# Optimization experiments

Hardware: AMD Instinct MI355X
Metric: run time of the kernel (lower is better)

The kernel has to match this reference:

```python
import jax, jax.numpy as jnp
import numpy as np

B, S, F = 512, 512, 128   # batch, seq_len, facts_size (= querry_size)
H1, H2 = 80, 40
PAD = float(-2**32 + 1)


def setup_inputs() -> dict:
    key = jax.random.key(0)
    ks = jax.random.split(key, 12)
    inp = {
        "query": jax.random.normal(ks[0], (B, F), jnp.float32),
        "facts": jax.random.normal(ks[1], (B, S, F), jnp.float32),
        "mask": jax.random.randint(ks[2], (B, S), 0, 2, jnp.int32),
        # mlp1: querry_size -> facts_size
        "W1": jax.random.normal(ks[3], (F, F), jnp.float32) / np.sqrt(F),
        "b1": jnp.zeros((F,), jnp.float32),
        # PReLU alpha (per-feature, init zeros)
        "alpha": jnp.zeros((F,), jnp.float32),
        # mlp2: 4*F -> 80
        "W2": jax.random.normal(ks[4], (4 * F, H1), jnp.float32) / np.sqrt(4 * F),
        "b2": jnp.zeros((H1,), jnp.float32),
        # mlp3: 80 -> 40
        "W3": jax.random.normal(ks[5], (H1, H2), jnp.float32) / np.sqrt(H1),
        "b3": jnp.zeros((H2,), jnp.float32),
        # mlp4: 40 -> 1
        "W4": jax.random.normal(ks[6], (H2, 1), jnp.float32) / np.sqrt(H2),
        "b4": jnp.zeros((1,), jnp.float32),
    }
    return inp


def reference(query, facts, mask, W1, b1, alpha, W2, b2, W3, b3, W4, b4):
    # mlp1 + PReLU on the query
    q = query @ W1 + b1                                   # [B, F]
    q = jnp.where(q >= 0, q, alpha * q)                   # PReLU, alpha per-feature
    # broadcast query over sequence (tile+reshape in the original)
    qs = jnp.broadcast_to(q[:, None, :], (q.shape[0], S, F))  # [B, S, F]
    din = jnp.concatenate([qs, facts, qs - facts, qs * facts], axis=-1)  # [B,S,4F]
    h1 = jax.nn.sigmoid(din @ W2 + b2)                    # [B, S, 80]
    h2 = jax.nn.sigmoid(h1 @ W3 + b3)                     # [B, S, 40]
    scores = (h2 @ W4 + b4)[..., 0][:, None, :]           # [B, 1, S]
    key_masks = (mask == 1)[:, None, :]                   # [B, 1, S]
    scores = jnp.where(key_masks, scores, PAD)
    scores = jax.nn.softmax(scores, axis=-1)              # softmax over seq
    out = jnp.einsum("bqs,bsf->bqf", scores, facts)       # [B, 1, F]  (mode SUM)
    return out
```

## Files before the change

kernel.cpp:

```cpp
#include <hip/hip_runtime.h>
#include <hip/hip_bf16.h>

typedef __bf16 bf16x8 __attribute__((ext_vector_type(8)));
typedef float  f32x4  __attribute__((ext_vector_type(4)));

#define WBT_STRIDE 136
#define H1_STRIDE  104
#define W3T_STRIDE 104

__global__ __launch_bounds__(512, 4)
void attn_fused(const float* __restrict__ query,
                const float* __restrict__ facts,
                const int*   __restrict__ mask,
                const float* __restrict__ W1, const float* __restrict__ b1,
                const float* __restrict__ alpha,
                const float* __restrict__ W2, const float* __restrict__ b2,
                const float* __restrict__ W3, const float* __restrict__ b3,
                const float* __restrict__ W4,
                float* __restrict__ out)
{
    __shared__ __align__(16) __bf16 WbT[80 * WBT_STRIDE];
    __shared__ __align__(16) __bf16 W3T[48 * W3T_STRIDE];
    __shared__ __align__(16) __bf16 h1all[128 * H1_STRIDE];
    __shared__ float qy[128], qs[128], qcs[80];
    __shared__ float qpart[4][128], qcp[4][80];
    __shared__ float w4s[48], b3s[48];
    __shared__ float outw[8 * 128];
    __shared__ float Zw[8];

    const int b = blockIdx.x, t = threadIdx.x;

    if (t < 128) qy[t] = query[b * 128 + t];
    for (int e = t; e < 48 * 96; e += 512) {
        int j = e / 96, k = e % 96;
        W3T[j * W3T_STRIDE + k] = (j < 40 && k < 80) ? (__bf16)W3[k * 40 + j]
                                                     : (__bf16)0.0f;
    }
    for (int e = t; e < 128 * 16; e += 512) {
        int r = e >> 4, c = 80 + (e & 15);
        h1all[r * H1_STRIDE + c] = (__bf16)0.0f;
    }
    if (t < 48) { w4s[t] = (t < 40) ? W4[t] : 0.f; b3s[t] = (t < 40) ? b3[t] : 0.f; }
    __syncthreads();

    {
        int j = t & 127, kh = t >> 7;
        float acc = (kh == 0) ? b1[j] : 0.f;
        const float* w1p = W1 + (kh * 32) * 128 + j;
        #pragma unroll 8
        for (int k = 0; k < 32; ++k) acc = fmaf(qy[kh * 32 + k], w1p[k * 128], acc);
        qpart[kh][j] = acc;
    }
    __syncthreads();
    if (t < 128) {
        float s = (qpart[0][t] + qpart[1][t]) + (qpart[2][t] + qpart[3][t]);
        qs[t] = (s >= 0.f) ? s : alpha[t] * s;
    }
    __syncthreads();

    if (t < 320) {
        int jj = t % 80, hh = t / 80;
        float acc = (hh == 0) ? b2[jj] : 0.f;
        #pragma unroll 8
        for (int k = hh * 32; k < hh * 32 + 32; ++k)
            acc = fmaf(qs[k], W2[k * 80 + jj] + W2[(256 + k) * 80 + jj], acc);
        qcp[hh][jj] = acc;
    }
    for (int e = t; e < 128 * 80; e += 512) {
        int k = e / 80, n = e - k * 80;
        float w = W2[(128 + k) * 80 + n] - W2[(256 + k) * 80 + n]
                + qs[k] * W2[(384 + k) * 80 + n];
        WbT[n * WBT_STRIDE + k] = (__bf16)w;
    }
    __syncthreads();
    if (t < 80) qcs[t] = (qcp[0][t] + qcp[1][t]) + (qcp[2][t] + qcp[3][t]);
    __syncthreads();

    const int wave = t >> 6, lane = t & 63, qd = lane >> 4, m = lane & 15;
    const float* fb = facts + (size_t)b * (512 * 128);
    const int*   mb = mask + b * 512;
    __bf16* h1w = &h1all[wave * 16 * H1_STRIDE];

    float oacc[4][8];
    #pragma unroll
    for (int kc = 0; kc < 4; ++kc)
        #pragma unroll
        for (int i = 0; i < 8; ++i) oacc[kc][i] = 0.f;
    float Zl = 0.f;

    for (int tile = 0; tile < 4; ++tile) {
        const int s0 = wave * 64 + tile * 16;
        const int mv = mb[s0 + m];

        f32x4 av[4][2];
        {
            const float* p0 = &fb[(size_t)(s0 + m) * 128 + qd * 8];
            #pragma unroll
            for (int kc = 0; kc < 4; ++kc) {
                av[kc][0] = *(const f32x4*)(p0 + kc * 32);
                av[kc][1] = *(const f32x4*)(p0 + kc * 32 + 4);
            }
        }
        bf16x8 af[4];
        #pragma unroll
        for (int kc = 0; kc < 4; ++kc)
            #pragma unroll
            for (int i = 0; i < 8; ++i)
                af[kc][i] = (__bf16)((i < 4) ? av[kc][0][i] : av[kc][1][i - 4]);

        #pragma unroll
        for (int ct = 0; ct < 5; ++ct) {
            f32x4 acc = {0.f, 0.f, 0.f, 0.f};
            #pragma unroll
            for (int kc = 0; kc < 4; ++kc) {
                bf16x8 bfr = *(const bf16x8*)&WbT[(ct * 16 + m) * WBT_STRIDE + kc * 32 + qd * 8];
                acc = __builtin_amdgcn_mfma_f32_16x16x32_bf16(af[kc], bfr, acc, 0, 0, 0);
            }
            const int col = ct * 16 + m;
            const float qc = qcs[col];
            #pragma unroll
            for (int r = 0; r < 4; ++r) {
                float x = acc[r] + qc;
                float h = __builtin_amdgcn_rcpf(1.0f + __expf(-x));
                h1w[(qd * 4 + r) * H1_STRIDE + col] = (__bf16)h;
            }
        }
        asm volatile("s_waitcnt lgkmcnt(0)" ::: "memory");

        bf16x8 a2[3];
        #pragma unroll
        for (int kc = 0; kc < 3; ++kc)
            a2[kc] = *(const bf16x8*)&h1w[m * H1_STRIDE + kc * 32 + qd * 8];
        float sc[4] = {0.f, 0.f, 0.f, 0.f};
        #pragma unroll
        for (int ct = 0; ct < 3; ++ct) {
            f32x4 acc2 = {0.f, 0.f, 0.f, 0.f};
            #pragma unroll
            for (int kc = 0; kc < 3; ++kc) {
                bf16x8 bfr = *(const bf16x8*)&W3T[(ct * 16 + m) * W3T_STRIDE + kc * 32 + qd * 8];
                acc2 = __builtin_amdgcn_mfma_f32_16x16x32_bf16(a2[kc], bfr, acc2, 0, 0, 0);
            }
            const int col = ct * 16 + m;
            const float w4v = w4s[col], b3v = b3s[col];
            #pragma unroll
            for (int r = 0; r < 4; ++r) {
                float h2 = __builtin_amdgcn_rcpf(1.0f + __expf(-(acc2[r] + b3v)));
                sc[r] = fmaf(h2, w4v, sc[r]);
            }
        }
        #pragma unroll
        for (int d = 1; d < 16; d <<= 1)
            #pragma unroll
            for (int r = 0; r < 4; ++r)
                sc[r] += __shfl_xor(sc[r], d);

        const int idx = ((((m >> 2) << 4) | m) << 2);
        float s0v = __int_as_float(__builtin_amdgcn_ds_bpermute(idx, __float_as_int(sc[0])));
        float s1v = __int_as_float(__builtin_amdgcn_ds_bpermute(idx, __float_as_int(sc[1])));
        float s2v = __int_as_float(__builtin_amdgcn_ds_bpermute(idx, __float_as_int(sc[2])));
        float s3v = __int_as_float(__builtin_amdgcn_ds_bpermute(idx, __float_as_int(sc[3])));
        const int rr = m & 3;
        float srow = (rr == 0) ? s0v : (rr == 1) ? s1v : (rr == 2) ? s2v : s3v;

        const float pm = (mv == 1) ? __expf(srow) : 0.f;
        Zl += pm;
        #pragma unroll
        for (int kc = 0; kc < 4; ++kc)
            #pragma unroll
            for (int i = 0; i < 4; ++i) {
                oacc[kc][i]     = fmaf(pm, av[kc][0][i], oacc[kc][i]);
                oacc[kc][i + 4] = fmaf(pm, av[kc][1][i], oacc[kc][i + 4]);
            }
    }

    #pragma unroll
    for (int d = 1; d < 16; d <<= 1) {
        #pragma unroll
        for (int kc = 0; kc < 4; ++kc)
            #pragma unroll
            for (int i = 0; i < 8; ++i)
                oacc[kc][i] += __shfl_xor(oacc[kc][i], d);
        Zl += __shfl_xor(Zl, d);
    }
    if (m == 0) {
        #pragma unroll
        for (int kc = 0; kc < 4; ++kc)
            #pragma unroll
            for (int i = 0; i < 8; ++i)
                outw[wave * 128 + kc * 32 + qd * 8 + i] = oacc[kc][i];
        if (lane == 0) Zw[wave] = Zl;
    }
    __syncthreads();

    if (t < 128) {
        float v = 0.f, Z = 0.f;
        #pragma unroll
        for (int w = 0; w < 8; ++w) { v += outw[w * 128 + t]; Z += Zw[w]; }
        out[b * 128 + t] = v / Z;
    }
}

extern "C" void kernel_launch(void* const* d_in, const int* in_sizes, int n_in,
                              void* d_out, int out_size, void* d_ws, size_t ws_size,
                              hipStream_t stream) {
    (void)in_sizes; (void)n_in; (void)d_ws; (void)ws_size; (void)out_size;
    const float* query = (const float*)d_in[0];
    const float* facts = (const float*)d_in[1];
    const int*   mask  = (const int*)d_in[2];
    const float* W1 = (const float*)d_in[3];
    const float* b1 = (const float*)d_in[4];
    const float* al = (const float*)d_in[5];
    const float* W2 = (const float*)d_in[6];
    const float* b2 = (const float*)d_in[7];
    const float* W3 = (const float*)d_in[8];
    const float* b3 = (const float*)d_in[9];
    const float* W4 = (const float*)d_in[10];
    const float* b4 = (const float*)d_in[11];
    (void)b4;
    attn_fused<<<dim3(512), dim3(512), 0, stream>>>(
        query, facts, mask, W1, b1, al, W2, b2, W3, b3, W4, (float*)d_out);
}
```

Measured before the change: 233.2 us.

## Prefetch facts tiles via register double-buffering and swizzle WbT LDS layout

The first facts tile and all mask values are loaded at kernel start, so they overlap the weight-preprocessing prologue. Inside the now fully unrolled tile loop, the next tile is loaded into a second register buffer and the weighted accumulation for the previous tile is deferred. The WbT LDS layout is XOR-swizzled by row to reduce bank conflicts on the MFMA B-operand reads. This doubles the facts register footprint, which may reduce occupancy under the 512x4 launch bounds or cause spills.

```diff
diff --git a/kernel.cpp b/kernel.cpp
--- a/kernel.cpp
+++ b/kernel.cpp
@@ -29,6 +29,22 @@
     __shared__ float Zw[8];
 
     const int b = blockIdx.x, t = threadIdx.x;
+    const int wave = t >> 6, lane = t & 63, qd = lane >> 4, m = lane & 15;
+    const float* fb = facts + (size_t)b * (512 * 128);
+    const int*   mb = mask + b * 512;
+
+    f32x4 av[2][4][2];
+    int mv[4];
+    {
+        const float* p0 = &fb[(size_t)(wave * 64 + m) * 128 + qd * 8];
+        #pragma unroll
+        for (int kc = 0; kc < 4; ++kc) {
+            av[0][kc][0] = *(const f32x4*)(p0 + kc * 32);
+            av[0][kc][1] = *(const f32x4*)(p0 + kc * 32 + 4);
+        }
+        #pragma unroll
+        for (int tl = 0; tl < 4; ++tl) mv[tl] = mb[wave * 64 + tl * 16 + m];
+    }
 
     if (t < 128) qy[t] = query[b * 128 + t];
     for (int e = t; e < 48 * 96; e += 512) {
@@ -70,15 +86,12 @@
         int k = e / 80, n = e - k * 80;
         float w = W2[(128 + k) * 80 + n] - W2[(256 + k) * 80 + n]
                 + qs[k] * W2[(384 + k) * 80 + n];
-        WbT[n * WBT_STRIDE + k] = (__bf16)w;
+        WbT[n * WBT_STRIDE + (((k >> 3) ^ (n & 3)) << 3) + (k & 7)] = (__bf16)w;
     }
     __syncthreads();
     if (t < 80) qcs[t] = (qcp[0][t] + qcp[1][t]) + (qcp[2][t] + qcp[3][t]);
     __syncthreads();
 
-    const int wave = t >> 6, lane = t & 63, qd = lane >> 4, m = lane & 15;
-    const float* fb = facts + (size_t)b * (512 * 128);
-    const int*   mb = mask + b * 512;
     __bf16* h1w = &h1all[wave * 16 * H1_STRIDE];
 
     float oacc[4][8];
@@ -87,42 +100,54 @@
         #pragma unroll
         for (int i = 0; i < 8; ++i) oacc[kc][i] = 0.f;
     float Zl = 0.f;
-
+    float pmprev = 0.f;
+
+    #pragma unroll
     for (int tile = 0; tile < 4; ++tile) {
-        const int s0 = wave * 64 + tile * 16;
-        const int mv = mb[s0 + m];
-
-        f32x4 av[4][2];
-        {
-            const float* p0 = &fb[(size_t)(s0 + m) * 128 + qd * 8];
+        const int p = tile & 1;
+
+        if (tile > 0) {
+            #pragma unroll
+            for (int kc = 0; kc < 4; ++kc)
+                #pragma unroll
+                for (int i = 0; i < 4; ++i) {
+                    oacc[kc][i]     = fmaf(pmprev, av[1 - p][kc][0][i], oacc[kc][i]);
+                    oacc[kc][i + 4] = fmaf(pmprev, av[1 - p][kc][1][i], oacc[kc][i + 4]);
+                }
+            Zl += pmprev;
+        }
+        if (tile < 3) {
+            const float* pn = &fb[(size_t)(wave * 64 + (tile + 1) * 16 + m) * 128 + qd * 8];
             #pragma unroll
             for (int kc = 0; kc < 4; ++kc) {
-                av[kc][0] = *(const f32x4*)(p0 + kc * 32);
-                av[kc][1] = *(const f32x4*)(p0 + kc * 32 + 4);
-            }
-        }
+                av[1 - p][kc][0] = *(const f32x4*)(pn + kc * 32);
+                av[1 - p][kc][1] = *(const f32x4*)(pn + kc * 32 + 4);
+            }
+        }
+
         bf16x8 af[4];
         #pragma unroll
         for (int kc = 0; kc < 4; ++kc)
             #pragma unroll
             for (int i = 0; i < 8; ++i)
-                af[kc][i] = (__bf16)((i < 4) ? av[kc][0][i] : av[kc][1][i - 4]);
+                af[kc][i] = (__bf16)((i < 4) ? av[p][kc][0][i] : av[p][kc][1][i - 4]);
 
         #pragma unroll
         for (int ct = 0; ct < 5; ++ct) {
             f32x4 acc = {0.f, 0.f, 0.f, 0.f};
+            const int n1 = ct * 16 + m;
             #pragma unroll
             for (int kc = 0; kc < 4; ++kc) {
-                bf16x8 bfr = *(const bf16x8*)&WbT[(ct * 16 + m) * WBT_STRIDE + kc * 32 + qd * 8];
+                bf16x8 bfr = *(const bf16x8*)
+                    &WbT[n1 * WBT_STRIDE + (((kc * 4 + qd) ^ (m & 3)) << 3)];
                 acc = __builtin_amdgcn_mfma_f32_16x16x32_bf16(af[kc], bfr, acc, 0, 0, 0);
             }
-            const int col = ct * 16 + m;
-            const float qc = qcs[col];
+            const float qc = qcs[n1];
             #pragma unroll
             for (int r = 0; r < 4; ++r) {
                 float x = acc[r] + qc;
                 float h = __builtin_amdgcn_rcpf(1.0f + __expf(-x));
-                h1w[(qd * 4 + r) * H1_STRIDE + col] = (__bf16)h;
+                h1w[(qd * 4 + r) * H1_STRIDE + n1] = (__bf16)h;
             }
         }
         asm volatile("s_waitcnt lgkmcnt(0)" ::: "memory");
@@ -162,16 +187,16 @@
         const int rr = m & 3;
         float srow = (rr == 0) ? s0v : (rr == 1) ? s1v : (rr == 2) ? s2v : s3v;
 
-        const float pm = (mv == 1) ? __expf(srow) : 0.f;
-        Zl += pm;
-        #pragma unroll
-        for (int kc = 0; kc < 4; ++kc)
-            #pragma unroll
-            for (int i = 0; i < 4; ++i) {
-                oacc[kc][i]     = fmaf(pm, av[kc][0][i], oacc[kc][i]);
-                oacc[kc][i + 4] = fmaf(pm, av[kc][1][i], oacc[kc][i + 4]);
-            }
-    }
+        pmprev = (mv[tile] == 1) ? __expf(srow) : 0.f;
+    }
+    #pragma unroll
+    for (int kc = 0; kc < 4; ++kc)
+        #pragma unroll
+        for (int i = 0; i < 4; ++i) {
+            oacc[kc][i]     = fmaf(pmprev, av[1][kc][0][i], oacc[kc][i]);
+            oacc[kc][i + 4] = fmaf(pmprev, av[1][kc][1][i], oacc[kc][i + 4]);
+        }
+    Zl += pmprev;
 
     #pragma unroll
     for (int d = 1; d < 16; d <<= 1) {
```

New measurement: 248.5 us. 1.07x slower.

## Split per-batch weight prep into separate kernel and restructure weighted-sum reduction

Applied to the files above, without the earlier changes.

Moves the query MLP, PReLU, folded W2 weight construction and W3 transpose into a prep kernel that writes per-batch bf16 weights to workspace, so the main kernel only copies them into LDS. The main kernel prefetches the first facts tile and the mask before the weight load. It now stores softmax numerators to shared memory and does the weighted sum of facts in a second pass over global memory, replacing the register accumulator and the long shuffle reduction. W3T is read from global instead of LDS. The cost is an extra launch, workspace traffic and a second read of facts, in exchange for less prologue work and lower register and shuffle pressure.

```diff
diff --git a/kernel.cpp b/kernel.cpp
--- a/kernel.cpp
+++ b/kernel.cpp
@@ -3,97 +3,144 @@
 
 typedef __bf16 bf16x8 __attribute__((ext_vector_type(8)));
 typedef float  f32x4  __attribute__((ext_vector_type(4)));
+typedef float  f32x2  __attribute__((ext_vector_type(2)));
 
 #define WBT_STRIDE 136
 #define H1_STRIDE  104
-#define W3T_STRIDE 104
+
+#define WS_WBT   0u
+#define WS_QC    10485760u
+#define WS_W3T   10649600u
+
+__global__ __launch_bounds__(256)
+void k1_prep(const float* __restrict__ query,
+             const float* __restrict__ W1, const float* __restrict__ b1,
+             const float* __restrict__ alpha,
+             const float* __restrict__ W2, const float* __restrict__ b2,
+             const float* __restrict__ W3,
+             unsigned char* __restrict__ ws)
+{
+    __shared__ float qy[128];
+    __shared__ float qpart[2][128];
+    __shared__ float qs[128];
+    __shared__ float qcp[2][80];
+
+    const int b = blockIdx.x, t = threadIdx.x;
+    __hip_bfloat16* wbt = (__hip_bfloat16*)(ws + WS_WBT);
+    float*          qcw = (float*)(ws + WS_QC);
+    __hip_bfloat16* w3t = (__hip_bfloat16*)(ws + WS_W3T);
+
+    if (t < 128) qy[t] = query[b * 128 + t];
+    __syncthreads();
+
+    {
+        const int j = t & 127, kh = t >> 7;
+        float acc = (kh == 0) ? b1[j] : 0.0f;
+        const float* w1p = W1 + (kh * 64) * 128 + j;
+        #pragma unroll 4
+        for (int k = 0; k < 64; ++k) acc = fmaf(qy[kh * 64 + k], w1p[k * 128], acc);
+        qpart[kh][j] = acc;
+    }
+    if (b == 0) {
+        for (int e = t; e < 48 * 96; e += 256) {
+            int j = e / 96, k = e % 96;
+            float v = (j < 40 && k < 80) ? W3[k * 40 + j] : 0.0f;
+            w3t[e] = __hip_bfloat16(v);
+        }
+    }
+    __syncthreads();
+    if (t < 128) {
+        float s = qpart[0][t] + qpart[1][t];
+        float a = alpha[t];
+        qs[t] = (s >= 0.0f) ? s : a * s;
+    }
+    __syncthreads();
+
+    if (t < 160) {
+        const int jj = (t < 80) ? t : t - 80;
+        const int hh = (t < 80) ? 0 : 1;
+        float acc = (hh == 0) ? b2[jj] : 0.0f;
+        #pragma unroll 4
+        for (int k = hh * 64; k < hh * 64 + 64; ++k)
+            acc = fmaf(qs[k], W2[k * 80 + jj] + W2[(256 + k) * 80 + jj], acc);
+        qcp[hh][jj] = acc;
+    }
+    for (int e = t; e < 80 * 16; e += 256) {
+        const int n = e >> 4, c = e & 15;
+        bf16x8 v;
+        #pragma unroll
+        for (int j = 0; j < 8; ++j) {
+            const int k = c * 8 + j;
+            float w = W2[(128 + k) * 80 + n] - W2[(256 + k) * 80 + n]
+                    + qs[k] * W2[(384 + k) * 80 + n];
+            v[j] = (__bf16)w;
+        }
+        *(bf16x8*)&wbt[(size_t)b * 10240 + n * 128 + c * 8] = v;
+    }
+    __syncthreads();
+    if (t < 80) qcw[b * 80 + t] = qcp[0][t] + qcp[1][t];
+}
 
 __global__ __launch_bounds__(512, 4)
-void attn_fused(const float* __restrict__ query,
-                const float* __restrict__ facts,
-                const int*   __restrict__ mask,
-                const float* __restrict__ W1, const float* __restrict__ b1,
-                const float* __restrict__ alpha,
-                const float* __restrict__ W2, const float* __restrict__ b2,
-                const float* __restrict__ W3, const float* __restrict__ b3,
-                const float* __restrict__ W4,
-                float* __restrict__ out)
+void k2_main(const float* __restrict__ facts,
+             const int*   __restrict__ mask,
+             const float* __restrict__ W4, const float* __restrict__ b3,
+             const unsigned char* __restrict__ ws,
+             float* __restrict__ out)
 {
     __shared__ __align__(16) __bf16 WbT[80 * WBT_STRIDE];
-    __shared__ __align__(16) __bf16 W3T[48 * W3T_STRIDE];
     __shared__ __align__(16) __bf16 h1all[128 * H1_STRIDE];
-    __shared__ float qy[128], qs[128], qcs[80];
-    __shared__ float qpart[4][128], qcp[4][80];
+    __shared__ float qcs[80];
     __shared__ float w4s[48], b3s[48];
-    __shared__ float outw[8 * 128];
+    __shared__ float scores[512];
     __shared__ float Zw[8];
 
     const int b = blockIdx.x, t = threadIdx.x;
-
-    if (t < 128) qy[t] = query[b * 128 + t];
-    for (int e = t; e < 48 * 96; e += 512) {
-        int j = e / 96, k = e % 96;
-        W3T[j * W3T_STRIDE + k] = (j < 40 && k < 80) ? (__bf16)W3[k * 40 + j]
-                                                     : (__bf16)0.0f;
+    const int wave = t >> 6, lane = t & 63, qd = lane >> 4, m = lane & 15;
+    const float* fb = facts + (size_t)b * (512 * 128);
+    const int*   mb = mask + b * 512;
+
+    const __hip_bfloat16* wbt_g = (const __hip_bfloat16*)(ws + WS_WBT) + (size_t)b * 10240;
+    const float*          qcw   = (const float*)(ws + WS_QC) + b * 80;
+    const __bf16*         w3t_g = (const __bf16*)(ws + WS_W3T);
+
+    f32x4 av0[4][2];
+    int mv[4];
+    {
+        const float* p0 = &fb[(size_t)(wave * 64 + m) * 128 + qd * 8];
+        #pragma unroll
+        for (int kc = 0; kc < 4; ++kc) {
+            av0[kc][0] = *(const f32x4*)(p0 + kc * 32);
+            av0[kc][1] = *(const f32x4*)(p0 + kc * 32 + 4);
+        }
+        #pragma unroll
+        for (int tl = 0; tl < 4; ++tl) mv[tl] = mb[wave * 64 + tl * 16 + m];
+    }
+
+    for (int e = t; e < 80 * 16; e += 512) {
+        const int n = e >> 4, c = e & 15;
+        bf16x8 v = *(const bf16x8*)&wbt_g[n * 128 + c * 8];
+        *(bf16x8*)&WbT[n * WBT_STRIDE + c * 8] = v;
     }
     for (int e = t; e < 128 * 16; e += 512) {
         int r = e >> 4, c = 80 + (e & 15);
         h1all[r * H1_STRIDE + c] = (__bf16)0.0f;
     }
+    if (t < 80) qcs[t] = qcw[t];
     if (t < 48) { w4s[t] = (t < 40) ? W4[t] : 0.f; b3s[t] = (t < 40) ? b3[t] : 0.f; }
     __syncthreads();
 
-    {
-        int j = t & 127, kh = t >> 7;
-        float acc = (kh == 0) ? b1[j] : 0.f;
-        const float* w1p = W1 + (kh * 32) * 128 + j;
-        #pragma unroll 8
-        for (int k = 0; k < 32; ++k) acc = fmaf(qy[kh * 32 + k], w1p[k * 128], acc);
-        qpart[kh][j] = acc;
-    }
-    __syncthreads();
-    if (t < 128) {
-        float s = (qpart[0][t] + qpart[1][t]) + (qpart[2][t] + qpart[3][t]);
-        qs[t] = (s >= 0.f) ? s : alpha[t] * s;
-    }
-    __syncthreads();
-
-    if (t < 320) {
-        int jj = t % 80, hh = t / 80;
-        float acc = (hh == 0) ? b2[jj] : 0.f;
-        #pragma unroll 8
-        for (int k = hh * 32; k < hh * 32 + 32; ++k)
-            acc = fmaf(qs[k], W2[k * 80 + jj] + W2[(256 + k) * 80 + jj], acc);
-        qcp[hh][jj] = acc;
-    }
-    for (int e = t; e < 128 * 80; e += 512) {
-        int k = e / 80, n = e - k * 80;
-        float w = W2[(128 + k) * 80 + n] - W2[(256 + k) * 80 + n]
-                + qs[k] * W2[(384 + k) * 80 + n];
-        WbT[n * WBT_STRIDE + k] = (__bf16)w;
-    }
-    __syncthreads();
-    if (t < 80) qcs[t] = (qcp[0][t] + qcp[1][t]) + (qcp[2][t] + qcp[3][t]);
-    __syncthreads();
-
-    const int wave = t >> 6, lane = t & 63, qd = lane >> 4, m = lane & 15;
-    const float* fb = facts + (size_t)b * (512 * 128);
-    const int*   mb = mask + b * 512;
     __bf16* h1w = &h1all[wave * 16 * H1_STRIDE];
 
-    float oacc[4][8];
     #pragma unroll
-    for (int kc = 0; kc < 4; ++kc)
-        #pragma unroll
-        for (int i = 0; i < 8; ++i) oacc[kc][i] = 0.f;
-    float Zl = 0.f;
-
     for (int tile = 0; tile < 4; ++tile) {
         const int s0 = wave * 64 + tile * 16;
-        const int mv = mb[s0 + m];
 
         f32x4 av[4][2];
-        {
+        if (tile == 0) {
+            #pragma unroll
+            for (int kc = 0; kc < 4; ++kc) { av[kc][0] = av0[kc][0]; av[kc][1] = av0[kc][1]; }
+        } else {
             const float* p0 = &fb[(size_t)(s0 + m) * 128 + qd * 8];
             #pragma unroll
             for (int kc = 0; kc < 4; ++kc) {
@@ -111,18 +158,18 @@
         #pragma unroll
         for (int ct = 0; ct < 5; ++ct) {
             f32x4 acc = {0.f, 0.f, 0.f, 0.f};
+            const int n1 = ct * 16 + m;
             #pragma unroll
             for (int kc = 0; kc < 4; ++kc) {
-                bf16x8 bfr = *(const bf16x8*)&WbT[(ct * 16 + m) * WBT_STRIDE + kc * 32 + qd * 8];
+                bf16x8 bfr = *(const bf16x8*)&WbT[n1 * WBT_STRIDE + kc * 32 + qd * 8];
                 acc = __builtin_amdgcn_mfma_f32_16x16x32_bf16(af[kc], bfr, acc, 0, 0, 0);
             }
-            const int col = ct * 16 + m;
-            const float qc = qcs[col];
+            const float qc = qcs[n1];
             #pragma unroll
             for (int r = 0; r < 4; ++r) {
                 float x = acc[r] + qc;
                 float h = __builtin_amdgcn_rcpf(1.0f + __expf(-x));
-                h1w[(qd * 4 + r) * H1_STRIDE + col] = (__bf16)h;
+                h1w[(qd * 4 + r) * H1_STRIDE + n1] = (__bf16)h;
             }
         }
         asm volatile("s_waitcnt lgkmcnt(0)" ::: "memory");
@@ -132,12 +179,12 @@
         for (int kc = 0; kc < 3; ++kc)
             a2[kc] = *(const bf16x8*)&h1w[m * H1_STRIDE + kc * 32 + qd * 8];
         float sc[4] = {0.f, 0.f, 0.f, 0.f};
-        #pragma unroll
+        #pragma unroll 1
         for (int ct = 0; ct < 3; ++ct) {
             f32x4 acc2 = {0.f, 0.f, 0.f, 0.f};
             #pragma unroll
             for (int kc = 0; kc < 3; ++kc) {
-                bf16x8 bfr = *(const bf16x8*)&W3T[(ct * 16 + m) * W3T_STRIDE + kc * 32 + qd * 8];
+                bf16x8 bfr = *(const bf16x8*)&w3t_g[(ct * 16 + m) * 96 + kc * 32 + qd * 8];
                 acc2 = __builtin_amdgcn_mfma_f32_16x16x32_bf16(a2[kc], bfr, acc2, 0, 0, 0);
             }
             const int col = ct * 16 + m;
@@ -162,48 +209,46 @@
         const int rr = m & 3;
         float srow = (rr == 0) ? s0v : (rr == 1) ? s1v : (rr == 2) ? s2v : s3v;
 
-        const float pm = (mv == 1) ? __expf(srow) : 0.f;
-        Zl += pm;
-        #pragma unroll
-        for (int kc = 0; kc < 4; ++kc)
-            #pragma unroll
-            for (int i = 0; i < 4; ++i) {
-                oacc[kc][i]     = fmaf(pm, av[kc][0][i], oacc[kc][i]);
-                oacc[kc][i + 4] = fmaf(pm, av[kc][1][i], oacc[kc][i + 4]);
-            }
-    }
-
+        const float pm = (mv[tile] == 1) ? __expf(srow) : 0.f;
+        if (lane < 16) scores[s0 + lane] = pm;
+    }
+    __syncthreads();
+
+    float z = scores[t];
     #pragma unroll
-    for (int d = 1; d < 16; d <<= 1) {
-        #pragma unroll
-        for (int kc = 0; kc < 4; ++kc)
-            #pragma unroll
-            for (int i = 0; i < 8; ++i)
-                oacc[kc][i] += __shfl_xor(oacc[kc][i], d);
-        Zl += __shfl_xor(Zl, d);
-    }
-    if (m == 0) {
-        #pragma unroll
-        for (int kc = 0; kc < 4; ++kc)
-            #pragma unroll
-            for (int i = 0; i < 8; ++i)
-                outw[wave * 128 + kc * 32 + qd * 8 + i] = oacc[kc][i];
-        if (lane == 0) Zw[wave] = Zl;
-    }
+    for (int d = 1; d < 64; d <<= 1) z += __shfl_xor(z, d);
+    if (lane == 0) Zw[wave] = z;
+
+    float a0 = 0.f, a1 = 0.f;
+    {
+        const float* rp = fb + (size_t)(wave * 64) * 128 + 2 * lane;
+        const float* pp = &scores[wave * 64];
+        #pragma unroll 8
+        for (int s = 0; s < 64; ++s) {
+            f32x2 v = *(const f32x2*)(rp + (size_t)s * 128);
+            const float p = pp[s];
+            a0 = fmaf(p, v[0], a0);
+            a1 = fmaf(p, v[1], a1);
+        }
+    }
+    float* outw = (float*)h1all;
+    __syncthreads();
+    outw[wave * 128 + 2 * lane]     = a0;
+    outw[wave * 128 + 2 * lane + 1] = a1;
     __syncthreads();
 
     if (t < 128) {
-        float v = 0.f, Z = 0.f;
-        #pragma unroll
-        for (int w = 0; w < 8; ++w) { v += outw[w * 128 + t]; Z += Zw[w]; }
-        out[b * 128 + t] = v / Z;
+        float Zg = 0.f, v = 0.f;
+        #pragma unroll
+        for (int w = 0; w < 8; ++w) { v += outw[w * 128 + t]; Zg += Zw[w]; }
+        out[b * 128 + t] = v / Zg;
     }
 }
 
 extern "C" void kernel_launch(void* const* d_in, const int* in_sizes, int n_in,
                               void* d_out, int out_size, void* d_ws, size_t ws_size,
                               hipStream_t stream) {
-    (void)in_sizes; (void)n_in; (void)d_ws; (void)ws_size; (void)out_size;
+    (void)in_sizes; (void)n_in; (void)ws_size; (void)out_size;
     const float* query = (const float*)d_in[0];
     const float* facts = (const float*)d_in[1];
     const int*   mask  = (const int*)d_in[2];
@@ -217,6 +262,8 @@
     const float* W4 = (const float*)d_in[10];
     const float* b4 = (const float*)d_in[11];
     (void)b4;
-    attn_fused<<<dim3(512), dim3(512), 0, stream>>>(
-        query, facts, mask, W1, b1, al, W2, b2, W3, b3, W4, (float*)d_out);
+    unsigned char* ws = (unsigned char*)d_ws;
+
+    k1_prep<<<dim3(512), dim3(256), 0, stream>>>(query, W1, b1, al, W2, b2, W3, ws);
+    k2_main<<<dim3(512), dim3(512), 0, stream>>>(facts, mask, W4, b3, ws, (float*)d_out);
 }
```

After: 274.4 us. 1.18x slower.
